# Kernel tuning notes

Hardware: AMD Instinct MI355X
Metric: run time of the kernel (lower is better)

## Reference

```python
import jax, jax.numpy as jnp
import numpy as np

N_NODES = 50000
N_EDGES = 400000
IN_DIM, HID, OUT_DIM = 24, 256, 12


def _sage_conv(x, src, dst, w_l, b_l, w_r, num_nodes):
    # PyG SAGEConv (aggr='mean', root_weight=True):
    #   out = lin_l(mean_{j in N(i)} x_j) + lin_r(x_i)
    msg = x[src]                                             # [E, H] gather
    s = jax.ops.segment_sum(msg, dst, num_segments=num_nodes)  # [N, H]
    cnt = jax.ops.segment_sum(jnp.ones((src.shape[0],), x.dtype), dst,
                              num_segments=num_nodes)          # [N]
    mean = s / jnp.maximum(cnt, 1.0)[:, None]
    return mean @ w_l + b_l + x @ w_r


def setup_inputs() -> dict:
    key = jax.random.key(0)
    ks = jax.random.split(key, 16)
    sc = 0.05
    inp = {
        "x": jax.random.normal(ks[0], (N_NODES, IN_DIM), jnp.float32),
        "edge_index": jax.random.randint(ks[1], (2, N_EDGES), 0, N_NODES, jnp.int64),
        # encoder: Linear(24,128) ReLU Linear(128,256) ReLU
        "enc_w1": sc * jax.random.normal(ks[2], (IN_DIM, HID // 2), jnp.float32),
        "enc_b1": jnp.zeros((HID // 2,), jnp.float32),
        "enc_w2": sc * jax.random.normal(ks[3], (HID // 2, HID), jnp.float32),
        "enc_b2": jnp.zeros((HID,), jnp.float32),
        # SAGEConv 1 / 2: lin_l (with bias) on aggregated, lin_r (no bias) on root
        "s1_wl": sc * jax.random.normal(ks[4], (HID, HID), jnp.float32),
        "s1_bl": jnp.zeros((HID,), jnp.float32),
        "s1_wr": sc * jax.random.normal(ks[5], (HID, HID), jnp.float32),
        "s2_wl": sc * jax.random.normal(ks[6], (HID, HID), jnp.float32),
        "s2_bl": jnp.zeros((HID,), jnp.float32),
        "s2_wr": sc * jax.random.normal(ks[7], (HID, HID), jnp.float32),
        # readout: Linear(256,128) ReLU Linear(128,12)
        "ro_w1": sc * jax.random.normal(ks[8], (HID, HID // 2), jnp.float32),
        "ro_b1": jnp.zeros((HID // 2,), jnp.float32),
        "ro_w2": sc * jax.random.normal(ks[9], (HID // 2, OUT_DIM), jnp.float32),
        "ro_b2": jnp.zeros((OUT_DIM,), jnp.float32),
    }
    return inp


def reference(x, edge_index, enc_w1, enc_b1, enc_w2, enc_b2,
              s1_wl, s1_bl, s1_wr, s2_wl, s2_bl, s2_wr,
              ro_w1, ro_b1, ro_w2, ro_b2):
    n = x.shape[0]
    src, dst = edge_index[0], edge_index[1]
    # encoder MLP
    h = jax.nn.relu(x @ enc_w1 + enc_b1)
    h = jax.nn.relu(h @ enc_w2 + enc_b2)
    # two SAGE layers with ReLU
    h = jax.nn.relu(_sage_conv(h, src, dst, s1_wl, s1_bl, s1_wr, n))
    h = jax.nn.relu(_sage_conv(h, src, dst, s2_wl, s2_bl, s2_wr, n))
    # readout MLP
    h = jax.nn.relu(h @ ro_w1 + ro_b1)
    return h @ ro_w2 + ro_b2
```

## Files before the change

### kernel.cpp

```cpp
#include <hip/hip_runtime.h>
#include <hip/hip_bf16.h>

#define N_NODES 50000
#define N_EDGES 400000
#define IN_DIM 24
#define HID 256
#define OUT_DIM 12

typedef _Float16 fp16_t;
typedef __attribute__((ext_vector_type(8))) _Float16 half8;
typedef __attribute__((ext_vector_type(4))) float f32x4;

__device__ __forceinline__ void gload_lds16(const void* g, void* l) {
    typedef __attribute__((address_space(3))) unsigned int u32_lds;
    typedef const __attribute__((address_space(1))) unsigned int u32_glb;
    __builtin_amdgcn_global_load_lds((u32_glb*)(unsigned long long)g,
                                     (u32_lds*)(unsigned int)(unsigned long long)l,
                                     16, 0, 0);
}

template<int K, int M, int ROWS>
__global__ __launch_bounds__(M) void lin_enc1(const float* __restrict__ X,
                                              const float* __restrict__ W,
                                              const float* __restrict__ b,
                                              fp16_t* __restrict__ Y, int N) {
    __shared__ float xs[ROWS][K];
    const int row0 = blockIdx.x * ROWS;
    const int tid = threadIdx.x;
    for (int i = tid; i < ROWS * K; i += M) {
        int r = i / K, k = i - r * K;
        int gr = row0 + r;
        xs[r][k] = (gr < N) ? X[(long long)gr * K + k] : 0.f;
    }
    __syncthreads();
    const int j = tid;
    float acc[ROWS];
    float bj = b[j];
#pragma unroll
    for (int r = 0; r < ROWS; ++r) acc[r] = bj;
    for (int k = 0; k < K; ++k) {
        float w = W[k * M + j];
#pragma unroll
        for (int r = 0; r < ROWS; ++r) acc[r] = fmaf(xs[r][k], w, acc[r]);
    }
#pragma unroll
    for (int r = 0; r < ROWS; ++r) {
        int gr = row0 + r;
        if (gr < N) {
            float v = fmaxf(acc[r], 0.f);
            Y[(size_t)gr * M + j] = (fp16_t)v;
        }
    }
}

__global__ __launch_bounds__(256) void wtrans_all(
    const float* __restrict__ enc_w2,
    const float* __restrict__ s1_wl, const float* __restrict__ s1_wr,
    const float* __restrict__ s2_wl, const float* __restrict__ s2_wr,
    const float* __restrict__ ro_w1,
    fp16_t* __restrict__ wtE,
    fp16_t* __restrict__ wtS1,
    fp16_t* __restrict__ wtS2,
    fp16_t* __restrict__ wtR,
    int* __restrict__ deg, int N) {
    const int sE = 256 * 128, sS = 256 * 512, sR = 128 * 256;
    int idx = blockIdx.x * blockDim.x + threadIdx.x;
    if (idx < N) deg[idx] = 0;
    float v; fp16_t* p; int o;
    if (idx < sE) {
        int j = idx / 128, k = idx - j * 128;
        v = enc_w2[(size_t)k * 256 + j]; p = wtE; o = idx;
    } else if (idx < sE + sS) {
        int t = idx - sE; int j = t / 512, k = t - j * 512;
        v = (k < 256) ? s1_wl[(size_t)k * 256 + j] : s1_wr[(size_t)(k - 256) * 256 + j];
        p = wtS1; o = t;
    } else if (idx < sE + 2 * sS) {
        int t = idx - sE - sS; int j = t / 512, k = t - j * 512;
        v = (k < 256) ? s2_wl[(size_t)k * 256 + j] : s2_wr[(size_t)(k - 256) * 256 + j];
        p = wtS2; o = t;
    } else if (idx < sE + 2 * sS + sR) {
        int t = idx - sE - 2 * sS; int j = t / 256, k = t - j * 256;
        v = ro_w1[(size_t)k * 128 + j]; p = wtR; o = t;
    } else return;
    p[o] = (fp16_t)v;
}

template<int K, int MODE, int BM, int BN, bool WH16, bool RELU>
__global__ __launch_bounds__((BM / 64) * (BN / 64) * 64, 4) void gemm_mfma(
    const fp16_t* __restrict__ A, const fp16_t* __restrict__ A2,
    const fp16_t* __restrict__ W,
    const float* __restrict__ bias,
    fp16_t* __restrict__ Yh,
    int N, int M) {
    constexpr int NWR = BM / 64;
    constexpr int NWC = BN / 64;
    constexpr int NT = NWR * NWC * 64;
    __shared__ __align__(16) fp16_t ldsA[BM * 32];
    __shared__ __align__(16) fp16_t ldsB[BN * 32];
    const int tid = threadIdx.x;
    const int r0 = blockIdx.x * BM;
    const int j0 = blockIdx.y * BN;
    const int w = tid >> 6, lane = tid & 63;
    const int wr = w / NWC, wc = w % NWC;
    const int lrow = lane & 15, lg = lane >> 4;

    f32x4 acc[4][4] = {};

    for (int kc = 0; kc < K; kc += 32) {
        __syncthreads();
        const fp16_t* pa;
        int ka, KA;
        if (MODE == 1) {
            KA = HID;
            if (kc >= HID) { pa = A2; ka = kc - HID; }
            else           { pa = A;  ka = kc; }
        } else {
            KA = K; pa = A; ka = kc;
        }
#pragma unroll
        for (int c = tid; c < BM * 4; c += NT) {
            int row = c >> 2, p = c & 3;
            int g = (p - (row >> 1)) & 3;
            int gr = r0 + row; if (gr > N - 1) gr = N - 1;
            gload_lds16(pa + (size_t)gr * KA + ka + g * 8,
                        (char*)ldsA + (size_t)c * 16);
        }
#pragma unroll
        for (int c = tid; c < BN * 4; c += NT) {
            int row = c >> 2, p = c & 3;
            int g = (p - (row >> 1)) & 3;
            gload_lds16(W + (size_t)(j0 + row) * K + kc + g * 8,
                        (char*)ldsB + (size_t)c * 16);
        }
        __syncthreads();

        half8 a[4], b[4];
#pragma unroll
        for (int f = 0; f < 4; ++f) {
            int ar = wr * 64 + f * 16 + lrow;
            int sa = (lg + (ar >> 1)) & 3;
            a[f] = *(const half8*)&ldsA[ar * 32 + sa * 8];
            int br = wc * 64 + f * 16 + lrow;
            int sb = (lg + (br >> 1)) & 3;
            b[f] = *(const half8*)&ldsB[br * 32 + sb * 8];
        }
#pragma unroll
        for (int fi = 0; fi < 4; ++fi)
#pragma unroll
            for (int fj = 0; fj < 4; ++fj)
                acc[fi][fj] = __builtin_amdgcn_mfma_f32_16x16x32_f16(a[fi], b[fj], acc[fi][fj], 0, 0, 0);
    }

#pragma unroll
    for (int fj = 0; fj < 4; ++fj) {
        int ocol = j0 + wc * 64 + fj * 16 + lrow;
        float bv = bias[ocol];
#pragma unroll
        for (int fi = 0; fi < 4; ++fi) {
#pragma unroll
            for (int r = 0; r < 4; ++r) {
                int orow = r0 + wr * 64 + fi * 16 + lg * 4 + r;
                if (orow < N) {
                    float v = acc[fi][fj][r] + bv;
                    if (RELU) v = fmaxf(v, 0.f);
                    if (WH16) Yh[(size_t)orow * M + ocol] = (fp16_t)v;
                }
            }
        }
    }
}

__global__ __launch_bounds__(256, 3) void gemm_ro(
    const fp16_t* __restrict__ A,
    const fp16_t* __restrict__ W,
    const float* __restrict__ b1,
    const float* __restrict__ W2,
    const float* __restrict__ b2,
    float* __restrict__ out, int N) {
    constexpr int K = 256;
    __shared__ __align__(16) fp16_t ldsA[128 * 32];
    __shared__ __align__(16) fp16_t ldsB[128 * 32];
    __shared__ __align__(16) fp16_t htile[128 * 128];
    __shared__ __align__(16) fp16_t w2t[16 * 128];
    const int tid = threadIdx.x;
    const int r0 = blockIdx.x * 128;
    const int w = tid >> 6, lane = tid & 63;
    const int wr = w >> 1, wc = w & 1;
    const int lrow = lane & 15, lg = lane >> 4;

    for (int i = tid; i < 16 * 128; i += 256) {
        int c = i >> 7, k = i & 127;
        w2t[i] = (c < 12) ? (fp16_t)W2[k * 12 + c] : (fp16_t)0.f;
    }

    f32x4 acc[4][4] = {};
    for (int kc = 0; kc < K; kc += 32) {
        __syncthreads();
#pragma unroll
        for (int c = tid; c < 128 * 4; c += 256) {
            int row = c >> 2, p = c & 3;
            int g = (p - (row >> 1)) & 3;
            int gr = r0 + row; if (gr > N - 1) gr = N - 1;
            gload_lds16(A + (size_t)gr * K + kc + g * 8, (char*)ldsA + (size_t)c * 16);
        }
#pragma unroll
        for (int c = tid; c < 128 * 4; c += 256) {
            int row = c >> 2, p = c & 3;
            int g = (p - (row >> 1)) & 3;
            gload_lds16(W + (size_t)row * K + kc + g * 8, (char*)ldsB + (size_t)c * 16);
        }
        __syncthreads();

        half8 a[4], b[4];
#pragma unroll
        for (int f = 0; f < 4; ++f) {
            int ar = wr * 64 + f * 16 + lrow;
            int sa = (lg + (ar >> 1)) & 3;
            a[f] = *(const half8*)&ldsA[ar * 32 + sa * 8];
            int br = wc * 64 + f * 16 + lrow;
            int sb = (lg + (br >> 1)) & 3;
            b[f] = *(const half8*)&ldsB[br * 32 + sb * 8];
        }
#pragma unroll
        for (int fi = 0; fi < 4; ++fi)
#pragma unroll
            for (int fj = 0; fj < 4; ++fj)
                acc[fi][fj] = __builtin_amdgcn_mfma_f32_16x16x32_f16(a[fi], b[fj], acc[fi][fj], 0, 0, 0);
    }

#pragma unroll
    for (int fj = 0; fj < 4; ++fj) {
        int ocol = wc * 64 + fj * 16 + lrow;
        float bv = b1[ocol];
        int q = ocol >> 3;
#pragma unroll
        for (int fi = 0; fi < 4; ++fi) {
#pragma unroll
            for (int r = 0; r < 4; ++r) {
                int orow = wr * 64 + fi * 16 + lg * 4 + r;
                float v = fmaxf(acc[fi][fj][r] + bv, 0.f);
                int phys = (q + (orow >> 1)) & 15;
                htile[orow * 128 + phys * 8 + (ocol & 7)] = (fp16_t)v;
            }
        }
    }
    __syncthreads();

    if (w < 2) {
        f32x4 accF[4] = {};
#pragma unroll
        for (int kt = 0; kt < 4; ++kt) {
            half8 bb = *(const half8*)&w2t[lrow * 128 + kt * 32 + lg * 8];
            half8 a[4];
#pragma unroll
            for (int f = 0; f < 4; ++f) {
                int ar = w * 64 + f * 16 + lrow;
                int q = kt * 4 + lg;
                int phys = (q + (ar >> 1)) & 15;
                a[f] = *(const half8*)&htile[ar * 128 + phys * 8];
            }
#pragma unroll
            for (int f = 0; f < 4; ++f)
                accF[f] = __builtin_amdgcn_mfma_f32_16x16x32_f16(a[f], bb, accF[f], 0, 0, 0);
        }
        if (lrow < OUT_DIM) {
            float bv = b2[lrow];
#pragma unroll
            for (int f = 0; f < 4; ++f) {
#pragma unroll
                for (int r = 0; r < 4; ++r) {
                    int orow = r0 + w * 64 + f * 16 + lg * 4 + r;
                    if (orow < N) out[(size_t)orow * OUT_DIM + lrow] = accF[f][r] + bv;
                }
            }
        }
    }
}

__global__ void deg_kernel(const int* __restrict__ dst, int* __restrict__ deg, int E) {
    int e = blockIdx.x * blockDim.x + threadIdx.x;
    if (e < E) atomicAdd(&deg[dst[e]], 1);
}

__global__ __launch_bounds__(256) void scan_local(const int* __restrict__ deg,
                                                  int* __restrict__ locincl,
                                                  int* __restrict__ bsum, int N) {
    const int t = threadIdx.x;
    const int i = blockIdx.x * 256 + t;
    int v = (i < N) ? deg[i] : 0;
    const int lane = t & 63;
    int x = v;
#pragma unroll
    for (int off = 1; off < 64; off <<= 1) {
        int y = __shfl_up(x, off, 64);
        if (lane >= off) x += y;
    }
    __shared__ int wsum[4];
    if (lane == 63) wsum[t >> 6] = x;
    __syncthreads();
    const int wid = t >> 6;
    int add = 0;
    for (int wI = 0; wI < wid; ++wI) add += wsum[wI];
    x += add;
    if (i < N) locincl[i] = x;
    if (t == 255) bsum[blockIdx.x] = x;
}

__global__ __launch_bounds__(256) void scan_final(const int* __restrict__ deg,
                                                  const int* __restrict__ locincl,
                                                  const int* __restrict__ bsum,
                                                  int* __restrict__ rowptr,
                                                  int* __restrict__ cursor,
                                                  int N, int E, int B) {
    __shared__ int red[4];
    const int t = threadIdx.x;
    int s = (t < blockIdx.x && t < B) ? bsum[t] : 0;
#pragma unroll
    for (int off = 32; off > 0; off >>= 1) s += __shfl_down(s, off, 64);
    if ((t & 63) == 0) red[t >> 6] = s;
    __syncthreads();
    int base = red[0] + red[1] + red[2] + red[3];
    const int i = blockIdx.x * 256 + t;
    if (i < N) {
        int excl = base + locincl[i] - deg[i];
        rowptr[i] = excl;
        cursor[i] = excl;
    }
    if (i == 0) rowptr[N] = E;
}

__global__ void scatter_kernel(const int* __restrict__ src, const int* __restrict__ dst,
                               int* __restrict__ cursor, int* __restrict__ esrc, int E) {
    int e = blockIdx.x * blockDim.x + threadIdx.x;
    if (e < E) {
        int pos = atomicAdd(&cursor[dst[e]], 1);
        esrc[pos] = src[e];
    }
}

__global__ __launch_bounds__(256) void agg_csr(const fp16_t* __restrict__ h,
                                               const int* __restrict__ rowptr,
                                               const int* __restrict__ esrc,
                                               fp16_t* __restrict__ mean, int N) {
    const int n = blockIdx.x * 4 + (threadIdx.x >> 6);
    if (n >= N) return;
    const int lane = threadIdx.x & 63;
    const int half = lane >> 5;
    const int l32 = lane & 31;
    const int r0 = rowptr[n];
    const int r1 = rowptr[n + 1];
    const int deg = r1 - r0;

    float acc[8];
#pragma unroll
    for (int j = 0; j < 8; ++j) acc[j] = 0.f;

    for (int e = r0 + half; e < r1; e += 2) {
        int s = esrc[e];
        half8 v = *(const half8*)&h[(size_t)s * HID + l32 * 8];
#pragma unroll
        for (int j = 0; j < 8; ++j) acc[j] += (float)v[j];
    }
#pragma unroll
    for (int j = 0; j < 8; ++j) acc[j] += __shfl(acc[j], lane ^ 32, 64);

    if (half == 0) {
        float inv = 1.0f / fmaxf((float)deg, 1.0f);
        half8 o;
#pragma unroll
        for (int j = 0; j < 8; ++j) o[j] = (fp16_t)(acc[j] * inv);
        *(half8*)&mean[(size_t)n * HID + l32 * 8] = o;
    }
}

extern "C" void kernel_launch(void* const* d_in, const int* in_sizes, int n_in,
                              void* d_out, int out_size, void* d_ws, size_t ws_size,
                              hipStream_t stream) {
    const float* x      = (const float*)d_in[0];
    const int*   eidx   = (const int*)d_in[1];
    const float* enc_w1 = (const float*)d_in[2];
    const float* enc_b1 = (const float*)d_in[3];
    const float* enc_w2 = (const float*)d_in[4];
    const float* enc_b2 = (const float*)d_in[5];
    const float* s1_wl  = (const float*)d_in[6];
    const float* s1_bl  = (const float*)d_in[7];
    const float* s1_wr  = (const float*)d_in[8];
    const float* s2_wl  = (const float*)d_in[9];
    const float* s2_bl  = (const float*)d_in[10];
    const float* s2_wr  = (const float*)d_in[11];
    const float* ro_w1  = (const float*)d_in[12];
    const float* ro_b1  = (const float*)d_in[13];
    const float* ro_w2  = (const float*)d_in[14];
    const float* ro_b2  = (const float*)d_in[15];
    float* out = (float*)d_out;

    const int N = N_NODES;
    const int E = N_EDGES;
    const int* src = eidx;
    const int* dst = eidx + E;

    char* ws = (char*)d_ws;
    size_t off = 0;
    auto alloc = [&](size_t bytes) { void* p = ws + off; off += (bytes + 255) & ~255ULL; return p; };
    int* deg     = (int*)alloc((size_t)N * 4);
    int* rowptr  = (int*)alloc((size_t)(N + 1) * 4);
    int* cursor  = (int*)alloc((size_t)N * 4);
    int* esrc    = (int*)alloc((size_t)E * 4);
    int* locincl = (int*)alloc((size_t)N * 4);
    int* bsum    = (int*)alloc((size_t)256 * 4);
    fp16_t* wtE  = (fp16_t*)alloc((size_t)256 * 128 * 2);
    fp16_t* wtS1 = (fp16_t*)alloc((size_t)256 * 512 * 2);
    fp16_t* wtS2 = (fp16_t*)alloc((size_t)256 * 512 * 2);
    fp16_t* wtR  = (fp16_t*)alloc((size_t)128 * 256 * 2);
    fp16_t* h0   = (fp16_t*)alloc((size_t)N * 128 * 2);
    fp16_t* hA   = (fp16_t*)alloc((size_t)N * HID * 2);
    fp16_t* hB   = (fp16_t*)alloc((size_t)N * HID * 2);
    fp16_t* mbuf = (fp16_t*)alloc((size_t)N * HID * 2);

    const int nb8 = (N + 7) / 8;
    const int gx128 = (N + 127) / 128;
    const int nbScan = (N + 255) / 256;
    const int nbAgg = (N + 3) / 4;
    const int wtTot = 256 * 128 + 2 * 256 * 512 + 128 * 256;

    wtrans_all<<<(wtTot + 255) / 256, 256, 0, stream>>>(
        enc_w2, s1_wl, s1_wr, s2_wl, s2_wr, ro_w1, wtE, wtS1, wtS2, wtR, deg, N);

    deg_kernel<<<(E + 255) / 256, 256, 0, stream>>>(dst, deg, E);
    scan_local<<<nbScan, 256, 0, stream>>>(deg, locincl, bsum, N);
    scan_final<<<nbScan, 256, 0, stream>>>(deg, locincl, bsum, rowptr, cursor, N, E, nbScan);
    scatter_kernel<<<(E + 255) / 256, 256, 0, stream>>>(src, dst, cursor, esrc, E);

    lin_enc1<IN_DIM, 128, 8><<<nb8, 128, 0, stream>>>(x, enc_w1, enc_b1, h0, N);
    gemm_mfma<128, 0, 128, 256, true, true><<<dim3(gx128, 1), 512, 0, stream>>>(
        h0, nullptr, wtE, enc_b2, hA, N, 256);

    agg_csr<<<nbAgg, 256, 0, stream>>>(hA, rowptr, esrc, mbuf, N);
    gemm_mfma<512, 1, 128, 256, true, true><<<dim3(gx128, 1), 512, 0, stream>>>(
        mbuf, hA, wtS1, s1_bl, hB, N, 256);

    agg_csr<<<nbAgg, 256, 0, stream>>>(hB, rowptr, esrc, mbuf, N);
    gemm_mfma<512, 1, 128, 256, true, true><<<dim3(gx128, 1), 512, 0, stream>>>(
        mbuf, hB, wtS2, s2_bl, hA, N, 256);

    gemm_ro<<<gx128, 256, 0, stream>>>(hA, wtR, ro_b1, ro_w2, ro_b2, out, N);
}
```

Measured before the change: 228.5 us.

## Merge weight prep with encoder layer 1, and encoder GEMM with degree count

Folds the weight transpose/convert kernel and the first encoder linear layer into one launch, where blocks branch on their index. It also merges the second encoder GEMM with the edge degree atomic count into a single launch. The goal is fewer kernel launches and letting independent work run at the same time on the GPU. In exchange the merged kernels carry the larger register and LDS footprint of the GEMM for the degree blocks, and the encoder layer now runs 256-thread blocks of 16 rows.

```diff
diff --git a/kernel.cpp b/kernel.cpp
--- a/kernel.cpp
+++ b/kernel.cpp
@@ -19,87 +19,21 @@
                                      16, 0, 0);
 }
 
-template<int K, int M, int ROWS>
-__global__ __launch_bounds__(M) void lin_enc1(const float* __restrict__ X,
-                                              const float* __restrict__ W,
-                                              const float* __restrict__ b,
-                                              fp16_t* __restrict__ Y, int N) {
-    __shared__ float xs[ROWS][K];
-    const int row0 = blockIdx.x * ROWS;
-    const int tid = threadIdx.x;
-    for (int i = tid; i < ROWS * K; i += M) {
-        int r = i / K, k = i - r * K;
-        int gr = row0 + r;
-        xs[r][k] = (gr < N) ? X[(long long)gr * K + k] : 0.f;
-    }
-    __syncthreads();
-    const int j = tid;
-    float acc[ROWS];
-    float bj = b[j];
-#pragma unroll
-    for (int r = 0; r < ROWS; ++r) acc[r] = bj;
-    for (int k = 0; k < K; ++k) {
-        float w = W[k * M + j];
-#pragma unroll
-        for (int r = 0; r < ROWS; ++r) acc[r] = fmaf(xs[r][k], w, acc[r]);
-    }
-#pragma unroll
-    for (int r = 0; r < ROWS; ++r) {
-        int gr = row0 + r;
-        if (gr < N) {
-            float v = fmaxf(acc[r], 0.f);
-            Y[(size_t)gr * M + j] = (fp16_t)v;
-        }
-    }
-}
-
-__global__ __launch_bounds__(256) void wtrans_all(
-    const float* __restrict__ enc_w2,
-    const float* __restrict__ s1_wl, const float* __restrict__ s1_wr,
-    const float* __restrict__ s2_wl, const float* __restrict__ s2_wr,
-    const float* __restrict__ ro_w1,
-    fp16_t* __restrict__ wtE,
-    fp16_t* __restrict__ wtS1,
-    fp16_t* __restrict__ wtS2,
-    fp16_t* __restrict__ wtR,
-    int* __restrict__ deg, int N) {
-    const int sE = 256 * 128, sS = 256 * 512, sR = 128 * 256;
-    int idx = blockIdx.x * blockDim.x + threadIdx.x;
-    if (idx < N) deg[idx] = 0;
-    float v; fp16_t* p; int o;
-    if (idx < sE) {
-        int j = idx / 128, k = idx - j * 128;
-        v = enc_w2[(size_t)k * 256 + j]; p = wtE; o = idx;
-    } else if (idx < sE + sS) {
-        int t = idx - sE; int j = t / 512, k = t - j * 512;
-        v = (k < 256) ? s1_wl[(size_t)k * 256 + j] : s1_wr[(size_t)(k - 256) * 256 + j];
-        p = wtS1; o = t;
-    } else if (idx < sE + 2 * sS) {
-        int t = idx - sE - sS; int j = t / 512, k = t - j * 512;
-        v = (k < 256) ? s2_wl[(size_t)k * 256 + j] : s2_wr[(size_t)(k - 256) * 256 + j];
-        p = wtS2; o = t;
-    } else if (idx < sE + 2 * sS + sR) {
-        int t = idx - sE - 2 * sS; int j = t / 256, k = t - j * 256;
-        v = ro_w1[(size_t)k * 128 + j]; p = wtR; o = t;
-    } else return;
-    p[o] = (fp16_t)v;
-}
-
 template<int K, int MODE, int BM, int BN, bool WH16, bool RELU>
-__global__ __launch_bounds__((BM / 64) * (BN / 64) * 64, 4) void gemm_mfma(
+__device__ __forceinline__ void gemm_body(
     const fp16_t* __restrict__ A, const fp16_t* __restrict__ A2,
     const fp16_t* __restrict__ W,
     const float* __restrict__ bias,
     fp16_t* __restrict__ Yh,
-    int N, int M) {
+    int N, int M, int bx, int by) {
     constexpr int NWR = BM / 64;
     constexpr int NWC = BN / 64;
     constexpr int NT = NWR * NWC * 64;
     __shared__ __align__(16) fp16_t ldsA[BM * 32];
     __shared__ __align__(16) fp16_t ldsB[BN * 32];
     const int tid = threadIdx.x;
-    const int r0 = blockIdx.x * BM;
-    const int j0 = blockIdx.y * BN;
+    const int r0 = bx * BM;
+    const int j0 = by * BN;
     const int w = tid >> 6, lane = tid & 63;
     const int wr = w / NWC, wc = w % NWC;
     const int lrow = lane & 15, lg = lane >> 4;
@@ -168,6 +102,98 @@
             }
         }
     }
+}
+
+__device__ __forceinline__ void enc1_body(const float* __restrict__ X,
+                                          const float* __restrict__ W,
+                                          const float* __restrict__ b,
+                                          fp16_t* __restrict__ Y, int N, int bx) {
+    __shared__ float xs[16][IN_DIM];
+    const int tid = threadIdx.x;
+    const int row0 = bx * 16;
+    for (int i = tid; i < 16 * IN_DIM; i += 256) {
+        int r = i / IN_DIM, k = i - r * IN_DIM;
+        int gr = row0 + r;
+        xs[r][k] = (gr < N) ? X[(size_t)gr * IN_DIM + k] : 0.f;
+    }
+    __syncthreads();
+    const int j = tid & 127;
+    const int rg = tid >> 7;
+    float acc[8];
+    float bj = b[j];
+#pragma unroll
+    for (int r = 0; r < 8; ++r) acc[r] = bj;
+    for (int k = 0; k < IN_DIM; ++k) {
+        float w = W[k * 128 + j];
+#pragma unroll
+        for (int r = 0; r < 8; ++r) acc[r] = fmaf(xs[rg * 8 + r][k], w, acc[r]);
+    }
+#pragma unroll
+    for (int r = 0; r < 8; ++r) {
+        int gr = row0 + rg * 8 + r;
+        if (gr < N) Y[(size_t)gr * 128 + j] = (fp16_t)fmaxf(acc[r], 0.f);
+    }
+}
+
+__global__ __launch_bounds__(256) void k_prep(
+    const float* __restrict__ enc_w2,
+    const float* __restrict__ s1_wl, const float* __restrict__ s1_wr,
+    const float* __restrict__ s2_wl, const float* __restrict__ s2_wr,
+    const float* __restrict__ ro_w1,
+    fp16_t* __restrict__ wtE, fp16_t* __restrict__ wtS1,
+    fp16_t* __restrict__ wtS2, fp16_t* __restrict__ wtR,
+    int* __restrict__ deg,
+    const float* __restrict__ X, const float* __restrict__ enc_w1,
+    const float* __restrict__ enc_b1, fp16_t* __restrict__ h0,
+    int N, int nbW) {
+    const int sE = 256 * 128, sS = 256 * 512, sR = 128 * 256;
+    if ((int)blockIdx.x < nbW) {
+        int idx = blockIdx.x * 256 + threadIdx.x;
+        if (idx < N) deg[idx] = 0;
+        float v; fp16_t* p; int o;
+        if (idx < sE) {
+            int j = idx / 128, k = idx - j * 128;
+            v = enc_w2[(size_t)k * 256 + j]; p = wtE; o = idx;
+        } else if (idx < sE + sS) {
+            int t = idx - sE; int j = t / 512, k = t - j * 512;
+            v = (k < 256) ? s1_wl[(size_t)k * 256 + j] : s1_wr[(size_t)(k - 256) * 256 + j];
+            p = wtS1; o = t;
+        } else if (idx < sE + 2 * sS) {
+            int t = idx - sE - sS; int j = t / 512, k = t - j * 512;
+            v = (k < 256) ? s2_wl[(size_t)k * 256 + j] : s2_wr[(size_t)(k - 256) * 256 + j];
+            p = wtS2; o = t;
+        } else if (idx < sE + 2 * sS + sR) {
+            int t = idx - sE - 2 * sS; int j = t / 256, k = t - j * 256;
+            v = ro_w1[(size_t)k * 128 + j]; p = wtR; o = t;
+        } else return;
+        p[o] = (fp16_t)v;
+    } else {
+        enc1_body(X, enc_w1, enc_b1, h0, N, blockIdx.x - nbW);
+    }
+}
+
+__global__ __launch_bounds__(512, 4) void k_encgemm_deg(
+    const fp16_t* __restrict__ h0, const fp16_t* __restrict__ wtE,
+    const float* __restrict__ enc_b2, fp16_t* __restrict__ hA,
+    const int* __restrict__ dst, int* __restrict__ deg,
+    int N, int E, int nbGemm) {
+    if ((int)blockIdx.x < nbGemm) {
+        gemm_body<128, 0, 128, 256, true, true>(h0, nullptr, wtE, enc_b2, hA, N, 256,
+                                                blockIdx.x, 0);
+    } else {
+        int e = (blockIdx.x - nbGemm) * 512 + threadIdx.x;
+        if (e < E) atomicAdd(&deg[dst[e]], 1);
+    }
+}
+
+template<int K, int MODE, int BM, int BN, bool WH16, bool RELU>
+__global__ __launch_bounds__((BM / 64) * (BN / 64) * 64, 4) void gemm_mfma(
+    const fp16_t* __restrict__ A, const fp16_t* __restrict__ A2,
+    const fp16_t* __restrict__ W,
+    const float* __restrict__ bias,
+    fp16_t* __restrict__ Yh,
+    int N, int M) {
+    gemm_body<K, MODE, BM, BN, WH16, RELU>(A, A2, W, bias, Yh, N, M, blockIdx.x, blockIdx.y);
 }
 
 __global__ __launch_bounds__(256, 3) void gemm_ro(
@@ -275,11 +301,6 @@
             }
         }
     }
-}
-
-__global__ void deg_kernel(const int* __restrict__ dst, int* __restrict__ deg, int E) {
-    int e = blockIdx.x * blockDim.x + threadIdx.x;
-    if (e < E) atomicAdd(&deg[dst[e]], 1);
 }
 
 __global__ __launch_bounds__(256) void scan_local(const int* __restrict__ deg,
@@ -417,24 +438,25 @@
     fp16_t* hB   = (fp16_t*)alloc((size_t)N * HID * 2);
     fp16_t* mbuf = (fp16_t*)alloc((size_t)N * HID * 2);
 
-    const int nb8 = (N + 7) / 8;
     const int gx128 = (N + 127) / 128;
     const int nbScan = (N + 255) / 256;
     const int nbAgg = (N + 3) / 4;
     const int wtTot = 256 * 128 + 2 * 256 * 512 + 128 * 256;
-
-    wtrans_all<<<(wtTot + 255) / 256, 256, 0, stream>>>(
-        enc_w2, s1_wl, s1_wr, s2_wl, s2_wr, ro_w1, wtE, wtS1, wtS2, wtR, deg, N);
-
-    deg_kernel<<<(E + 255) / 256, 256, 0, stream>>>(dst, deg, E);
+    const int nbW = (wtTot + 255) / 256;
+    const int nbEnc = (N + 15) / 16;
+    const int nbDeg512 = (E + 511) / 512;
+
+    k_prep<<<nbW + nbEnc, 256, 0, stream>>>(
+        enc_w2, s1_wl, s1_wr, s2_wl, s2_wr, ro_w1,
+        wtE, wtS1, wtS2, wtR, deg, x, enc_w1, enc_b1, h0, N, nbW);
+
+    k_encgemm_deg<<<gx128 + nbDeg512, 512, 0, stream>>>(
+        h0, wtE, enc_b2, hA, dst, deg, N, E, gx128);
+
     scan_local<<<nbScan, 256, 0, stream>>>(deg, locincl, bsum, N);
     scan_final<<<nbScan, 256, 0, stream>>>(deg, locincl, bsum, rowptr, cursor, N, E, nbScan);
     scatter_kernel<<<(E + 255) / 256, 256, 0, stream>>>(src, dst, cursor, esrc, E);
 
-    lin_enc1<IN_DIM, 128, 8><<<nb8, 128, 0, stream>>>(x, enc_w1, enc_b1, h0, N);
-    gemm_mfma<128, 0, 128, 256, true, true><<<dim3(gx128, 1), 512, 0, stream>>>(
-        h0, nullptr, wtE, enc_b2, hA, N, 256);
-
     agg_csr<<<nbAgg, 256, 0, stream>>>(hA, rowptr, esrc, mbuf, N);
     gemm_mfma<512, 1, 128, 256, true, true><<<dim3(gx128, 1), 512, 0, stream>>>(
         mbuf, hA, wtS1, s1_bl, hB, N, 256);
```

After: 221.4 us, median of 2. 1.03x faster.
